# Kernel tuning notes

Measured on AMD Instinct MI355X. Metric: run time of the kernel, lower is better.

Reference implementation:

```python
import jax, jax.numpy as jnp
import numpy as np

D_MODEL = 1024
D_KEY = 64
BATCH = 4
SEQ = 4096


def setup_inputs() -> dict:
    key = jax.random.key(0)
    kq, kk, kv, kwq, kwk, kwv = jax.random.split(key, 6)
    queries = jax.random.normal(kq, (BATCH, SEQ, D_MODEL), dtype=jnp.float32)
    keys = jax.random.normal(kk, (BATCH, SEQ, D_MODEL), dtype=jnp.float32)
    values = jax.random.normal(kv, (BATCH, SEQ, D_MODEL), dtype=jnp.float32)
    # causal mask: 1 = keep, 0 = masked out (torch masked_fill where mask==0)
    mask = jnp.tril(jnp.ones((SEQ, SEQ), dtype=jnp.int32))
    s = 1.0 / np.sqrt(D_MODEL)
    Wq = jax.random.normal(kwq, (D_MODEL, D_KEY), dtype=jnp.float32) * s
    Wk = jax.random.normal(kwk, (D_MODEL, D_KEY), dtype=jnp.float32) * s
    Wv = jax.random.normal(kwv, (D_MODEL, D_KEY), dtype=jnp.float32) * s
    return {"queries": queries, "keys": keys, "values": values,
            "mask": mask, "Wq": Wq, "Wk": Wk, "Wv": Wv}


def reference(queries, keys, values, mask, Wq, Wk, Wv):
    q = jnp.einsum('bsd,dk->bsk', queries, Wq)   # [B,S,dk]
    k = jnp.einsum('bsd,dk->bsk', keys, Wk)
    v = jnp.einsum('bsd,dk->bsk', values, Wv)
    scale = 1.0 / np.sqrt(D_KEY).astype(np.float32)
    attn = jnp.einsum('bqk,bsk->bqs', q, k) * scale  # [B,Sq,Sk]
    attn = jnp.where(mask == 0, -jnp.inf, attn)
    attn = jax.nn.softmax(attn, axis=-1)
    return jnp.einsum('bqs,bsk->bqk', attn, v)      # [B,S,dk]
```

## Files before the change

kernel.cpp:

```cpp
#include <hip/hip_runtime.h>
#include <hip/hip_bf16.h>

#define B      4
#define SEQ    4096
#define DM     1024
#define DK     64
#define NSPLIT 8

typedef __bf16 bf16x8 __attribute__((ext_vector_type(8)));
typedef __bf16 bf16x4 __attribute__((ext_vector_type(4)));
typedef float  f32x4  __attribute__((ext_vector_type(4)));

#define KSTR 72

#define QSCALE 0.1803368801111204f
#define M2BIAS 12.0f

__global__ __launch_bounds__(256) void wt_kernel(
    const float* __restrict__ Wq, const float* __restrict__ Wk,
    const float* __restrict__ Wv, __bf16* __restrict__ Wt)
{
    const int mat = blockIdx.y;
    const float* W = (mat == 0) ? Wq : (mat == 1) ? Wk : Wv;
    const float scale = (mat == 0) ? QSCALE : 1.0f;
    const int k0 = blockIdx.x * 64;
    const int tid = threadIdx.x;

    __shared__ float t[64][65];

    const int r = tid >> 2;
    const int c = (tid & 3) * 16;
    {
        const float* src = W + (size_t)(k0 + r) * DK + c;
        #pragma unroll
        for (int j = 0; j < 4; ++j) {
            float4 a = *(const float4*)(src + j * 4);
            t[r][c + j * 4 + 0] = a.x; t[r][c + j * 4 + 1] = a.y;
            t[r][c + j * 4 + 2] = a.z; t[r][c + j * 4 + 3] = a.w;
        }
    }
    __syncthreads();
    const int n  = tid >> 2;
    const int kk = (tid & 3) * 16;
    bf16x8 b0, b1;
    #pragma unroll
    for (int j = 0; j < 8; ++j) b0[j] = (__bf16)(t[kk + j][n] * scale);
    #pragma unroll
    for (int j = 0; j < 8; ++j) b1[j] = (__bf16)(t[kk + 8 + j][n] * scale);
    __bf16* dst = Wt + (size_t)(mat * DK + n) * DM + k0 + kk;
    *(bf16x8*)(dst)     = b0;
    *(bf16x8*)(dst + 8) = b1;
}

#define DA 8
#define DW 4
__global__ __launch_bounds__(256) void proj_stream_kernel(
    const float* __restrict__ q_in, const float* __restrict__ k_in,
    const float* __restrict__ v_in, const __bf16* __restrict__ Wt,
    __bf16* __restrict__ qb, __bf16* __restrict__ kb,
    __bf16* __restrict__ vtb)
{
    const int m = blockIdx.y;
    const float* in = (m == 0) ? q_in : (m == 1) ? k_in : v_in;
    const __bf16* wt = Wt + (size_t)m * DK * DM;

    const int rowbase = blockIdx.x * 64;
    const int tid  = threadIdx.x;
    const int w    = tid >> 6;
    const int lane = tid & 63;
    const int quad = lane >> 4;
    const int l15  = lane & 15;

    const float*  arow = in + (size_t)(rowbase + w * 16 + l15) * DM + quad * 8;
    const __bf16* wrow = wt + (size_t)l15 * DM + quad * 8;

    float4 Aa[DA], Ab[DA];
    bf16x8 Wb[DW][4];
    #pragma unroll
    for (int d = 0; d < DA; ++d) {
        const float* ap = arow + d * 32;
        Aa[d] = *(const float4*)(ap);
        Ab[d] = *(const float4*)(ap + 4);
    }
    #pragma unroll
    for (int d = 0; d < DW; ++d) {
        const __bf16* wp = wrow + d * 32;
        Wb[d][0] = *(const bf16x8*)(wp);
        Wb[d][1] = *(const bf16x8*)(wp + 16 * DM);
        Wb[d][2] = *(const bf16x8*)(wp + 32 * DM);
        Wb[d][3] = *(const bf16x8*)(wp + 48 * DM);
    }

    f32x4 acc[4];
    #pragma unroll
    for (int nf = 0; nf < 4; ++nf) acc[nf] = (f32x4){0.f, 0.f, 0.f, 0.f};

    #pragma unroll
    for (int it = 0; it < 32; ++it) {
        const int da = it & (DA - 1);
        const int dw = it & (DW - 1);
        bf16x8 af;
        af[0] = (__bf16)Aa[da].x; af[1] = (__bf16)Aa[da].y;
        af[2] = (__bf16)Aa[da].z; af[3] = (__bf16)Aa[da].w;
        af[4] = (__bf16)Ab[da].x; af[5] = (__bf16)Ab[da].y;
        af[6] = (__bf16)Ab[da].z; af[7] = (__bf16)Ab[da].w;
        acc[0] = __builtin_amdgcn_mfma_f32_16x16x32_bf16(af, Wb[dw][0], acc[0], 0, 0, 0);
        acc[1] = __builtin_amdgcn_mfma_f32_16x16x32_bf16(af, Wb[dw][1], acc[1], 0, 0, 0);
        acc[2] = __builtin_amdgcn_mfma_f32_16x16x32_bf16(af, Wb[dw][2], acc[2], 0, 0, 0);
        acc[3] = __builtin_amdgcn_mfma_f32_16x16x32_bf16(af, Wb[dw][3], acc[3], 0, 0, 0);
        if (it + DA < 32) {
            const float* ap = arow + (it + DA) * 32;
            Aa[da] = *(const float4*)(ap);
            Ab[da] = *(const float4*)(ap + 4);
        }
        if (it + DW < 32) {
            const __bf16* wp = wrow + (it + DW) * 32;
            Wb[dw][0] = *(const bf16x8*)(wp);
            Wb[dw][1] = *(const bf16x8*)(wp + 16 * DM);
            Wb[dw][2] = *(const bf16x8*)(wp + 32 * DM);
            Wb[dw][3] = *(const bf16x8*)(wp + 48 * DM);
        }
    }

    if (m < 2) {
        __bf16* outb = (m == 0) ? qb : kb;
        #pragma unroll
        for (int nf = 0; nf < 4; ++nf)
            #pragma unroll
            for (int r = 0; r < 4; ++r)
                outb[(size_t)(rowbase + w * 16 + quad * 4 + r) * DK + nf * 16 + l15] =
                    (__bf16)acc[nf][r];
    } else {
        const int bb = rowbase >> 12;
        const int s0 = (rowbase & (SEQ - 1)) + w * 16 + quad * 4;
        #pragma unroll
        for (int nf = 0; nf < 4; ++nf) {
            bf16x4 v4;
            #pragma unroll
            for (int r = 0; r < 4; ++r) v4[r] = (__bf16)acc[nf][r];
            *(bf16x4*)&vtb[(size_t)(bb * DK + nf * 16 + l15) * SEQ + s0] = v4;
        }
    }
}

__global__ __launch_bounds__(256) void flash_kernel(
    const __bf16* __restrict__ qb, const __bf16* __restrict__ kb,
    const __bf16* __restrict__ vtb, __bf16* __restrict__ Opart,
    float* __restrict__ lpart)
{
    const int qt  = blockIdx.x;
    const int bb  = blockIdx.y;
    const int z   = blockIdx.z;
    const int tid = threadIdx.x;
    const int w    = tid >> 6;
    const int lane = tid & 63;
    const int quad = lane >> 4;
    const int l15  = lane & 15;

    __shared__ __bf16 Ks[64 * KSTR];
    __shared__ __bf16 Vs[64 * KSTR];
    __shared__ __bf16 Ps[4][2][16 * KSTR];

    const int qrow_base = qt * 128 + w * 32;
    const int niters = 2 * qt + 2;
    const int kt0 = (niters * z) / NSPLIT;
    const int kt1 = (niters * (z + 1)) / NSPLIT;

    bf16x8 qf[2][2];
    #pragma unroll
    for (int g = 0; g < 2; ++g) {
        const __bf16* qp = qb + ((size_t)(bb * SEQ + qrow_base + g * 16 + l15)) * DK + quad * 8;
        qf[g][0] = *(const bf16x8*)(qp);
        qf[g][1] = *(const bf16x8*)(qp + 32);
    }

    bf16x8 ones;
    #pragma unroll
    for (int j = 0; j < 8; ++j) ones[j] = (__bf16)1.0f;

    f32x4 of[2][4], lacc[2];
    #pragma unroll
    for (int g = 0; g < 2; ++g) {
        #pragma unroll
        for (int nf = 0; nf < 4; ++nf) of[g][nf] = (f32x4){0.f, 0.f, 0.f, 0.f};
        lacc[g] = (f32x4){0.f, 0.f, 0.f, 0.f};
    }

    const int sr = tid >> 2;
    const int sc = (tid & 3) * 16;
    bf16x8 kr0, kr1, vr0, vr1;
    const __bf16* kbase = kb  + ((size_t)(bb * SEQ + sr)) * DK + sc;
    const __bf16* vbase = vtb + ((size_t)(bb * DK  + sr)) * SEQ + sc;

    if (kt1 > kt0) {
        const __bf16* kg = kbase + (size_t)kt0 * 64 * DK;
        kr0 = *(const bf16x8*)(kg); kr1 = *(const bf16x8*)(kg + 8);
        const __bf16* vg = vbase + kt0 * 64;
        vr0 = *(const bf16x8*)(vg); vr1 = *(const bf16x8*)(vg + 8);
    }

    for (int kt = kt0; kt < kt1; ++kt) {
        __syncthreads();
        *(bf16x8*)&Ks[sr * KSTR + sc]     = kr0;
        *(bf16x8*)&Ks[sr * KSTR + sc + 8] = kr1;
        *(bf16x8*)&Vs[sr * KSTR + sc]     = vr0;
        *(bf16x8*)&Vs[sr * KSTR + sc + 8] = vr1;
        __syncthreads();
        if (kt + 1 < kt1) {
            const __bf16* kg = kbase + (size_t)(kt + 1) * 64 * DK;
            kr0 = *(const bf16x8*)(kg); kr1 = *(const bf16x8*)(kg + 8);
            const __bf16* vg = vbase + (kt + 1) * 64;
            vr0 = *(const bf16x8*)(vg); vr1 = *(const bf16x8*)(vg + 8);
        }

        f32x4 sf[2][4];
        #pragma unroll
        for (int g = 0; g < 2; ++g)
            #pragma unroll
            for (int nf = 0; nf < 4; ++nf)
                sf[g][nf] = (f32x4){-M2BIAS, -M2BIAS, -M2BIAS, -M2BIAS};
        #pragma unroll
        for (int nf = 0; nf < 4; ++nf) {
            #pragma unroll
            for (int ch = 0; ch < 2; ++ch) {
                bf16x8 kf = *(const bf16x8*)(&Ks[(nf * 16 + l15) * KSTR + ch * 32 + quad * 8]);
                sf[0][nf] = __builtin_amdgcn_mfma_f32_16x16x32_bf16(qf[0][ch], kf, sf[0][nf], 0, 0, 0);
                sf[1][nf] = __builtin_amdgcn_mfma_f32_16x16x32_bf16(qf[1][ch], kf, sf[1][nf], 0, 0, 0);
            }
        }

        const int kc0 = kt * 64;
        #pragma unroll
        for (int g = 0; g < 2; ++g) {
            const int r0 = qrow_base + g * 16;
            const bool dg = (kc0 + 63 > r0);
            #pragma unroll
            for (int nf = 0; nf < 4; ++nf) {
                #pragma unroll
                for (int r = 0; r < 4; ++r) {
                    float s = sf[g][nf][r];
                    if (dg) {
                        const int col = kc0 + nf * 16 + l15;
                        const int row = r0 + quad * 4 + r;
                        if (col > row) s = -1.0e9f;
                    }
                    const float p = __builtin_amdgcn_exp2f(s);
                    Ps[w][g][(quad * 4 + r) * KSTR + nf * 16 + l15] = (__bf16)p;
                }
            }
        }

        bf16x8 pf[2][2];
        #pragma unroll
        for (int g = 0; g < 2; ++g) {
            pf[g][0] = *(const bf16x8*)(&Ps[w][g][l15 * KSTR + quad * 8]);
            pf[g][1] = *(const bf16x8*)(&Ps[w][g][l15 * KSTR + 32 + quad * 8]);
            lacc[g] = __builtin_amdgcn_mfma_f32_16x16x32_bf16(pf[g][0], ones, lacc[g], 0, 0, 0);
            lacc[g] = __builtin_amdgcn_mfma_f32_16x16x32_bf16(pf[g][1], ones, lacc[g], 0, 0, 0);
        }

        #pragma unroll
        for (int nf = 0; nf < 4; ++nf) {
            #pragma unroll
            for (int ch = 0; ch < 2; ++ch) {
                bf16x8 vf = *(const bf16x8*)(&Vs[(nf * 16 + l15) * KSTR + ch * 32 + quad * 8]);
                of[0][nf] = __builtin_amdgcn_mfma_f32_16x16x32_bf16(pf[0][ch], vf, of[0][nf], 0, 0, 0);
                of[1][nf] = __builtin_amdgcn_mfma_f32_16x16x32_bf16(pf[1][ch], vf, of[1][nf], 0, 0, 0);
            }
        }
    }

    #pragma unroll
    for (int g = 0; g < 2; ++g) {
        __bf16* Op = Opart + ((size_t)(z * B + bb) * SEQ + qrow_base + g * 16) * DK;
        #pragma unroll
        for (int nf = 0; nf < 4; ++nf)
            #pragma unroll
            for (int r = 0; r < 4; ++r)
                Op[(size_t)(quad * 4 + r) * DK + nf * 16 + l15] = (__bf16)of[g][nf][r];
        if (l15 == 0) {
            const size_t base = (size_t)(z * B + bb) * SEQ + qrow_base + g * 16 + quad * 4;
            #pragma unroll
            for (int r = 0; r < 4; ++r)
                lpart[base + r] = lacc[g][r];
        }
    }
}

__global__ __launch_bounds__(256) void combine_kernel(
    const __bf16* __restrict__ Opart, const float* __restrict__ lpart,
    float* __restrict__ out)
{
    const int idx = blockIdx.x * 256 + threadIdx.x;
    const int row = idx >> 6;

    float L = 0.f, o = 0.f;
    #pragma unroll
    for (int z = 0; z < NSPLIT; ++z) {
        L += lpart[(size_t)z * (B * SEQ) + row];
        o += (float)Opart[(size_t)z * (B * SEQ) * DK + idx];
    }
    out[idx] = o / L;
}

extern "C" void kernel_launch(void* const* d_in, const int* in_sizes, int n_in,
                              void* d_out, int out_size, void* d_ws, size_t ws_size,
                              hipStream_t stream)
{
    const float* queries = (const float*)d_in[0];
    const float* keys    = (const float*)d_in[1];
    const float* values  = (const float*)d_in[2];
    const float* Wq = (const float*)d_in[4];
    const float* Wk = (const float*)d_in[5];
    const float* Wv = (const float*)d_in[6];
    float* out = (float*)d_out;

    char* p = (char*)d_ws;
    __bf16* qb  = (__bf16*)p;  p += (size_t)B * SEQ * DK * 2;
    __bf16* kb  = (__bf16*)p;  p += (size_t)B * SEQ * DK * 2;
    __bf16* vtb = (__bf16*)p;  p += (size_t)B * SEQ * DK * 2;
    __bf16* Wt  = (__bf16*)p;  p += (size_t)3 * DK * DM * 2;
    __bf16* Opart = (__bf16*)p; p += (size_t)NSPLIT * B * SEQ * DK * 2;
    float* lpart = (float*)p;   p += (size_t)NSPLIT * B * SEQ * 4;

    wt_kernel<<<dim3(DM / 64, 3), 256, 0, stream>>>(Wq, Wk, Wv, Wt);

    proj_stream_kernel<<<dim3((B * SEQ) / 64, 3), 256, 0, stream>>>(
        queries, keys, values, Wt, qb, kb, vtb);

    flash_kernel<<<dim3(SEQ / 128, B, NSPLIT), 256, 0, stream>>>(
        qb, kb, vtb, Opart, lpart);

    combine_kernel<<<(B * SEQ * DK) / 256, 256, 0, stream>>>(
        Opart, lpart, out);
}
```

Baseline: 290.8 us.

## Split projection K dimension across waves and drop flash LDS staging of K/V

The projection kernel now handles 16-row strips per block. It stages the fp32 inputs as bf16 in shared memory, and each wave reduces a quarter of the model dimension, with a cross-wave sum through shared memory. The flash kernel no longer stages K and V tiles in LDS behind block barriers; each wave loads its MFMA operands directly from global memory. This removes the barriers and LDS traffic in the attention loop, but it repeats K/V global loads across the four waves and loses the previous prefetch overlap.

Result: slower. 317.8 us (+9.3%).

```diff
diff --git a/kernel.cpp b/kernel.cpp
--- a/kernel.cpp
+++ b/kernel.cpp
@@ -12,6 +12,7 @@
 typedef float  f32x4  __attribute__((ext_vector_type(4)));
 
 #define KSTR 72
+#define ASTR 1032
 
 #define QSCALE 0.1803368801111204f
 #define M2BIAS 12.0f
@@ -52,9 +53,7 @@
     *(bf16x8*)(dst + 8) = b1;
 }
 
-#define DA 8
-#define DW 4
-__global__ __launch_bounds__(256) void proj_stream_kernel(
+__global__ __launch_bounds__(256) void proj_strip_kernel(
     const float* __restrict__ q_in, const float* __restrict__ k_in,
     const float* __restrict__ v_in, const __bf16* __restrict__ Wt,
     __bf16* __restrict__ qb, __bf16* __restrict__ kb,
@@ -64,82 +63,80 @@
     const float* in = (m == 0) ? q_in : (m == 1) ? k_in : v_in;
     const __bf16* wt = Wt + (size_t)m * DK * DM;
 
-    const int rowbase = blockIdx.x * 64;
+    const int rowbase = blockIdx.x * 16;
     const int tid  = threadIdx.x;
     const int w    = tid >> 6;
     const int lane = tid & 63;
     const int quad = lane >> 4;
     const int l15  = lane & 15;
 
-    const float*  arow = in + (size_t)(rowbase + w * 16 + l15) * DM + quad * 8;
-    const __bf16* wrow = wt + (size_t)l15 * DM + quad * 8;
-
-    float4 Aa[DA], Ab[DA];
-    bf16x8 Wb[DW][4];
-    #pragma unroll
-    for (int d = 0; d < DA; ++d) {
-        const float* ap = arow + d * 32;
-        Aa[d] = *(const float4*)(ap);
-        Ab[d] = *(const float4*)(ap + 4);
-    }
-    #pragma unroll
-    for (int d = 0; d < DW; ++d) {
-        const __bf16* wp = wrow + d * 32;
-        Wb[d][0] = *(const bf16x8*)(wp);
-        Wb[d][1] = *(const bf16x8*)(wp + 16 * DM);
-        Wb[d][2] = *(const bf16x8*)(wp + 32 * DM);
-        Wb[d][3] = *(const bf16x8*)(wp + 48 * DM);
-    }
+    __shared__ char SM[16 * ASTR * 2];
+    __bf16* As = (__bf16*)SM;
+    float*  Rs = (float*)SM;
+
+    const float* src = in + (size_t)rowbase * DM;
+    float4 ld[16];
+    #pragma unroll
+    for (int i = 0; i < 16; ++i)
+        ld[i] = *(const float4*)(src + i * 1024 + tid * 4);
+    #pragma unroll
+    for (int i = 0; i < 16; ++i) {
+        bf16x4 b;
+        b[0] = (__bf16)ld[i].x; b[1] = (__bf16)ld[i].y;
+        b[2] = (__bf16)ld[i].z; b[3] = (__bf16)ld[i].w;
+        *(bf16x4*)&As[i * ASTR + tid * 4] = b;
+    }
+    __syncthreads();
 
     f32x4 acc[4];
     #pragma unroll
     for (int nf = 0; nf < 4; ++nf) acc[nf] = (f32x4){0.f, 0.f, 0.f, 0.f};
 
-    #pragma unroll
-    for (int it = 0; it < 32; ++it) {
-        const int da = it & (DA - 1);
-        const int dw = it & (DW - 1);
-        bf16x8 af;
-        af[0] = (__bf16)Aa[da].x; af[1] = (__bf16)Aa[da].y;
-        af[2] = (__bf16)Aa[da].z; af[3] = (__bf16)Aa[da].w;
-        af[4] = (__bf16)Ab[da].x; af[5] = (__bf16)Ab[da].y;
-        af[6] = (__bf16)Ab[da].z; af[7] = (__bf16)Ab[da].w;
-        acc[0] = __builtin_amdgcn_mfma_f32_16x16x32_bf16(af, Wb[dw][0], acc[0], 0, 0, 0);
-        acc[1] = __builtin_amdgcn_mfma_f32_16x16x32_bf16(af, Wb[dw][1], acc[1], 0, 0, 0);
-        acc[2] = __builtin_amdgcn_mfma_f32_16x16x32_bf16(af, Wb[dw][2], acc[2], 0, 0, 0);
-        acc[3] = __builtin_amdgcn_mfma_f32_16x16x32_bf16(af, Wb[dw][3], acc[3], 0, 0, 0);
-        if (it + DA < 32) {
-            const float* ap = arow + (it + DA) * 32;
-            Aa[da] = *(const float4*)(ap);
-            Ab[da] = *(const float4*)(ap + 4);
-        }
-        if (it + DW < 32) {
-            const __bf16* wp = wrow + (it + DW) * 32;
-            Wb[dw][0] = *(const bf16x8*)(wp);
-            Wb[dw][1] = *(const bf16x8*)(wp + 16 * DM);
-            Wb[dw][2] = *(const bf16x8*)(wp + 32 * DM);
-            Wb[dw][3] = *(const bf16x8*)(wp + 48 * DM);
-        }
-    }
+    const int kbase = w * 256;
+    #pragma unroll
+    for (int j = 0; j < 8; ++j) {
+        const int kc = kbase + j * 32;
+        bf16x8 af = *(const bf16x8*)&As[l15 * ASTR + kc + quad * 8];
+        #pragma unroll
+        for (int nf = 0; nf < 4; ++nf) {
+            bf16x8 wb = *(const bf16x8*)(wt + (size_t)(nf * 16 + l15) * DM + kc + quad * 8);
+            acc[nf] = __builtin_amdgcn_mfma_f32_16x16x32_bf16(af, wb, acc[nf], 0, 0, 0);
+        }
+    }
+    __syncthreads();
+
+    #pragma unroll
+    for (int nf = 0; nf < 4; ++nf)
+        #pragma unroll
+        for (int r = 0; r < 4; ++r)
+            Rs[(w * 16 + quad * 4 + r) * 64 + nf * 16 + l15] = acc[nf][r];
+    __syncthreads();
 
     if (m < 2) {
         __bf16* outb = (m == 0) ? qb : kb;
-        #pragma unroll
-        for (int nf = 0; nf < 4; ++nf)
-            #pragma unroll
-            for (int r = 0; r < 4; ++r)
-                outb[(size_t)(rowbase + w * 16 + quad * 4 + r) * DK + nf * 16 + l15] =
-                    (__bf16)acc[nf][r];
+        const int c  = tid & 63;
+        const int r0 = tid >> 6;
+        #pragma unroll
+        for (int rr = 0; rr < 4; ++rr) {
+            const int r = r0 + rr * 4;
+            const float o = Rs[r * 64 + c] + Rs[1024 + r * 64 + c] +
+                            Rs[2048 + r * 64 + c] + Rs[3072 + r * 64 + c];
+            outb[(size_t)(rowbase + r) * DK + c] = (__bf16)o;
+        }
     } else {
+        const int c2 = tid >> 2;
+        const int x  = tid & 3;
         const int bb = rowbase >> 12;
-        const int s0 = (rowbase & (SEQ - 1)) + w * 16 + quad * 4;
-        #pragma unroll
-        for (int nf = 0; nf < 4; ++nf) {
-            bf16x4 v4;
-            #pragma unroll
-            for (int r = 0; r < 4; ++r) v4[r] = (__bf16)acc[nf][r];
-            *(bf16x4*)&vtb[(size_t)(bb * DK + nf * 16 + l15) * SEQ + s0] = v4;
-        }
+        const int s0 = rowbase & (SEQ - 1);
+        bf16x4 v4;
+        #pragma unroll
+        for (int y = 0; y < 4; ++y) {
+            const int s = x * 4 + y;
+            const float o = Rs[s * 64 + c2] + Rs[1024 + s * 64 + c2] +
+                            Rs[2048 + s * 64 + c2] + Rs[3072 + s * 64 + c2];
+            v4[y] = (__bf16)o;
+        }
+        *(bf16x4*)&vtb[(size_t)(bb * DK + c2) * SEQ + s0 + x * 4] = v4;
     }
 }
 
@@ -157,8 +154,6 @@
     const int quad = lane >> 4;
     const int l15  = lane & 15;
 
-    __shared__ __bf16 Ks[64 * KSTR];
-    __shared__ __bf16 Vs[64 * KSTR];
     __shared__ __bf16 Ps[4][2][16 * KSTR];
 
     const int qrow_base = qt * 128 + w * 32;
@@ -186,31 +181,16 @@
         lacc[g] = (f32x4){0.f, 0.f, 0.f, 0.f};
     }
 
-    const int sr = tid >> 2;
-    const int sc = (tid & 3) * 16;
-    bf16x8 kr0, kr1, vr0, vr1;
-    const __bf16* kbase = kb  + ((size_t)(bb * SEQ + sr)) * DK + sc;
-    const __bf16* vbase = vtb + ((size_t)(bb * DK  + sr)) * SEQ + sc;
-
-    if (kt1 > kt0) {
-        const __bf16* kg = kbase + (size_t)kt0 * 64 * DK;
-        kr0 = *(const bf16x8*)(kg); kr1 = *(const bf16x8*)(kg + 8);
-        const __bf16* vg = vbase + kt0 * 64;
-        vr0 = *(const bf16x8*)(vg); vr1 = *(const bf16x8*)(vg + 8);
-    }
+    const __bf16* kB = kb  + (size_t)bb * SEQ * DK + (size_t)l15 * DK + quad * 8;
+    const __bf16* vB = vtb + (size_t)bb * DK * SEQ + (size_t)l15 * SEQ + quad * 8;
 
     for (int kt = kt0; kt < kt1; ++kt) {
-        __syncthreads();
-        *(bf16x8*)&Ks[sr * KSTR + sc]     = kr0;
-        *(bf16x8*)&Ks[sr * KSTR + sc + 8] = kr1;
-        *(bf16x8*)&Vs[sr * KSTR + sc]     = vr0;
-        *(bf16x8*)&Vs[sr * KSTR + sc + 8] = vr1;
-        __syncthreads();
-        if (kt + 1 < kt1) {
-            const __bf16* kg = kbase + (size_t)(kt + 1) * 64 * DK;
-            kr0 = *(const bf16x8*)(kg); kr1 = *(const bf16x8*)(kg + 8);
-            const __bf16* vg = vbase + (kt + 1) * 64;
-            vr0 = *(const bf16x8*)(vg); vr1 = *(const bf16x8*)(vg + 8);
+        bf16x8 kf[4][2];
+        #pragma unroll
+        for (int nf = 0; nf < 4; ++nf) {
+            const __bf16* kp = kB + (size_t)(kt * 64 + nf * 16) * DK;
+            kf[nf][0] = *(const bf16x8*)(kp);
+            kf[nf][1] = *(const bf16x8*)(kp + 32);
         }
 
         f32x4 sf[2][4];
@@ -223,10 +203,17 @@
         for (int nf = 0; nf < 4; ++nf) {
             #pragma unroll
             for (int ch = 0; ch < 2; ++ch) {
-                bf16x8 kf = *(const bf16x8*)(&Ks[(nf * 16 + l15) * KSTR + ch * 32 + quad * 8]);
-                sf[0][nf] = __builtin_amdgcn_mfma_f32_16x16x32_bf16(qf[0][ch], kf, sf[0][nf], 0, 0, 0);
-                sf[1][nf] = __builtin_amdgcn_mfma_f32_16x16x32_bf16(qf[1][ch], kf, sf[1][nf], 0, 0, 0);
+                sf[0][nf] = __builtin_amdgcn_mfma_f32_16x16x32_bf16(qf[0][ch], kf[nf][ch], sf[0][nf], 0, 0, 0);
+                sf[1][nf] = __builtin_amdgcn_mfma_f32_16x16x32_bf16(qf[1][ch], kf[nf][ch], sf[1][nf], 0, 0, 0);
             }
+        }
+
+        bf16x8 vf[4][2];
+        #pragma unroll
+        for (int nf = 0; nf < 4; ++nf) {
+            const __bf16* vp = vB + (size_t)(nf * 16) * SEQ + kt * 64;
+            vf[nf][0] = *(const bf16x8*)(vp);
+            vf[nf][1] = *(const bf16x8*)(vp + 32);
         }
 
         const int kc0 = kt * 64;
@@ -263,9 +250,8 @@
         for (int nf = 0; nf < 4; ++nf) {
             #pragma unroll
             for (int ch = 0; ch < 2; ++ch) {
-                bf16x8 vf = *(const bf16x8*)(&Vs[(nf * 16 + l15) * KSTR + ch * 32 + quad * 8]);
-                of[0][nf] = __builtin_amdgcn_mfma_f32_16x16x32_bf16(pf[0][ch], vf, of[0][nf], 0, 0, 0);
-                of[1][nf] = __builtin_amdgcn_mfma_f32_16x16x32_bf16(pf[1][ch], vf, of[1][nf], 0, 0, 0);
+                of[0][nf] = __builtin_amdgcn_mfma_f32_16x16x32_bf16(pf[0][ch], vf[nf][ch], of[0][nf], 0, 0, 0);
+                of[1][nf] = __builtin_amdgcn_mfma_f32_16x16x32_bf16(pf[1][ch], vf[nf][ch], of[1][nf], 0, 0, 0);
             }
         }
     }
@@ -325,7 +311,7 @@
 
     wt_kernel<<<dim3(DM / 64, 3), 256, 0, stream>>>(Wq, Wk, Wv, Wt);
 
-    proj_stream_kernel<<<dim3((B * SEQ) / 64, 3), 256, 0, stream>>>(
+    proj_strip_kernel<<<dim3((B * SEQ) / 16, 3), 256, 0, stream>>>(
         queries, keys, values, Wt, qb, kb, vtb);
 
     flash_kernel<<<dim3(SEQ / 128, B, NSPLIT), 256, 0, stream>>>(
```
